# Optimization experiments

Hardware: AMD Instinct MI355X
Metric: run time of the kernel (lower is better)

## Reference

```python
import jax, jax.numpy as jnp
import numpy as np

N_NODES = 50000
N_EDGES = 800000
D = 64


def setup_inputs() -> dict:
    key = jax.random.key(0)
    k = jax.random.split(key, 8)
    h = jax.random.normal(k[0], (N_NODES, D), dtype=jnp.float32)
    edge_src = jax.random.randint(k[1], (N_EDGES,), 0, N_NODES, dtype=jnp.int32)
    edge_dst = jax.random.randint(k[2], (N_EDGES,), 0, N_NODES, dtype=jnp.int32)
    # normalized adjacency weights (e.g. 1/deg style values in (0,1))
    edge_w = jax.random.uniform(k[3], (N_EDGES,), dtype=jnp.float32)
    W_self = jax.random.normal(k[4], (D, D), dtype=jnp.float32) / np.sqrt(D)
    b_self = jnp.zeros((D,), dtype=jnp.float32)
    W_neigh = jax.random.normal(k[5], (D, D), dtype=jnp.float32) / np.sqrt(D)
    b_neigh = jnp.zeros((D,), dtype=jnp.float32)
    return {
        "h": h,
        "edge_src": edge_src,
        "edge_dst": edge_dst,
        "edge_w": edge_w,
        "W_self": W_self,
        "b_self": b_self,
        "W_neigh": W_neigh,
        "b_neigh": b_neigh,
    }


def reference(h, edge_src, edge_dst, edge_w, W_self, b_self, W_neigh, b_neigh):
    # neigh = A_norm @ h : sparse COO matmul as weighted gather + segment-sum
    # messages: [E, D]
    msgs = edge_w[:, None] * h[edge_src]
    neigh = jax.ops.segment_sum(msgs, edge_dst, num_segments=N_NODES)  # [N, D]
    # out = lin_self(h) + lin_neigh(neigh), relu; dropout is a no-op in eval mode
    out = (h @ W_self.T + b_self) + (neigh @ W_neigh.T + b_neigh)
    return jax.nn.relu(out)
```

## Files before the change

kernel.cpp:

```cpp
#include <hip/hip_runtime.h>

#define N_NODES 50000
#define N_EDGES 800000
#define D 64

#define NPB 200
#define NB  250
#define CAP 4096
#define BT  256
#define EPT 8
#define CHUNK_E (BT * EPT)
#define NCHUNKS ((N_EDGES + CHUNK_E - 1) / CHUNK_E)
#define CT  512

typedef unsigned short ushort_t;
typedef unsigned int   uint_t;

__device__ __forceinline__ ushort_t f2b(float f) {
    uint_t u = __float_as_uint(f);
    return (ushort_t)((u + 0x7FFFu + ((u >> 16) & 1u)) >> 16);
}
__device__ __forceinline__ float b2f(ushort_t b) {
    return __uint_as_float((uint_t)b << 16);
}


__global__ __launch_bounds__(256) void init_cursor_kernel(int* __restrict__ cursor)
{
    const int t = threadIdx.x;
    if (t < NB) cursor[t] = t * CAP;
}

__global__ __launch_bounds__(256) void h2b_kernel(
    const float* __restrict__ h, ushort_t* __restrict__ hb)
{
    const int i = blockIdx.x * 256 + threadIdx.x;
    if (i >= N_NODES * D / 4) return;
    const float4 v = ((const float4*)h)[i];
    ushort4 o;
    o.x = f2b(v.x); o.y = f2b(v.y); o.z = f2b(v.z); o.w = f2b(v.w);
    ((ushort4*)hb)[i] = o;
}

__global__ __launch_bounds__(BT) void bin_kernel(
    const int* __restrict__ src, const int* __restrict__ dst,
    const float* __restrict__ w, int* __restrict__ cursor,
    int2* __restrict__ bedges)
{
    __shared__ int lh[NB];
    __shared__ int loff[NB];
    __shared__ int lcur[NB];
    __shared__ int gpos[NB];
    __shared__ int part[256];
    __shared__ int2 stage[CHUNK_E];
    __shared__ unsigned char sbk[CHUNK_E];

    const int t = threadIdx.x;
    for (int i = t; i < NB; i += BT) lh[i] = 0;
    __syncthreads();

    const int base = blockIdx.x * CHUNK_E;
    int   my_b[EPT];
    int   my_p[EPT];
    float my_w[EPT];
#pragma unroll
    for (int k = 0; k < EPT; ++k) {
        const int e = base + k * BT + t;
        if (e < N_EDGES) {
            const int d = dst[e];
            const int b = (unsigned)d / NPB;
            my_b[k] = b;
            my_p[k] = (src[e] << 8) | (d - b * NPB);
            my_w[k] = w[e];
            atomicAdd(&lh[b], 1);
        } else {
            my_b[k] = -1;
        }
    }
    __syncthreads();

    const int v = (t < NB) ? lh[t] : 0;
    part[t] = v;
    __syncthreads();
    for (int off = 1; off < 256; off <<= 1) {
        int p = (t >= off) ? part[t - off] : 0;
        __syncthreads();
        part[t] += p;
        __syncthreads();
    }
    if (t < NB) { loff[t] = part[t] - v; lcur[t] = part[t] - v; }
    __syncthreads();

#pragma unroll
    for (int k = 0; k < EPT; ++k) {
        if (my_b[k] >= 0) {
            const int p = atomicAdd(&lcur[my_b[k]], 1);
            stage[p] = make_int2(my_p[k], __float_as_int(my_w[k]));
            sbk[p] = (unsigned char)my_b[k];
        }
    }
    __syncthreads();

    if (t < NB && lh[t] > 0) gpos[t] = atomicAdd(&cursor[t], lh[t]);
    __syncthreads();

    const int tot = min(N_EDGES - base, CHUNK_E);
    for (int s = t; s < tot; s += BT) {
        const int b = sbk[s];
        bedges[gpos[b] + (s - loff[b])] = stage[s];
    }
}

__global__ __launch_bounds__(CT) void bucket_csr_kernel(
    const int* __restrict__ cursor, int2* __restrict__ edges,
    int2* __restrict__ offs2)
{
    __shared__ int  lcur[NPB];
    __shared__ int  part[256];
    __shared__ int2 stage[CAP];

    const int b   = blockIdx.x;
    const int t   = threadIdx.x;
    const int gb  = b * CAP;
    const int cnt = min(cursor[b] - gb, CAP);

    if (t < NPB) lcur[t] = 0;
    __syncthreads();
    for (int e = t; e < cnt; e += CT)
        atomicAdd(&lcur[edges[gb + e].x & 255], 1);
    __syncthreads();

    const int v = (t < NPB) ? lcur[t] : 0;
    if (t < 256) part[t] = v;
    __syncthreads();
    for (int off = 1; off < 256; off <<= 1) {
        int p = (t >= off && t < 256) ? part[t - off] : 0;
        __syncthreads();
        if (t < 256) part[t] += p;
        __syncthreads();
    }
    if (t < NPB) {
        const int ex = part[t] - v;
        lcur[t] = ex;
        offs2[b * NPB + t] = make_int2(gb + ex, gb + ex + v);
    }
    __syncthreads();

    for (int e = t; e < cnt; e += CT) {
        const int2 r = edges[gb + e];
        const int p = atomicAdd(&lcur[r.x & 255], 1);
        stage[p] = make_int2(r.x >> 8, r.y);
    }
    __syncthreads();
    for (int s = t; s < cnt; s += CT)
        edges[gb + s] = stage[s];
}

__global__ __launch_bounds__(256) void gather_kernel(
    const ushort_t* __restrict__ hb, const int2* __restrict__ edges,
    const int2* __restrict__ offs2, ushort_t* __restrict__ neigh)
{
    const int node = (blockIdx.x * 256 + threadIdx.x) >> 6;
    const int lane = threadIdx.x & 63;
    if (node >= N_NODES) return;
    const int2 be = offs2[node];
    const int beg = be.x, end = be.y;
    float acc = 0.f;
    int e = beg;
    for (; e + 4 <= end; e += 4) {
        const int2 e0 = edges[e], e1 = edges[e + 1], e2 = edges[e + 2], e3 = edges[e + 3];
        const float v0 = b2f(hb[(size_t)e0.x * D + lane]);
        const float v1 = b2f(hb[(size_t)e1.x * D + lane]);
        const float v2 = b2f(hb[(size_t)e2.x * D + lane]);
        const float v3 = b2f(hb[(size_t)e3.x * D + lane]);
        acc = fmaf(__int_as_float(e0.y), v0, acc);
        acc = fmaf(__int_as_float(e1.y), v1, acc);
        acc = fmaf(__int_as_float(e2.y), v2, acc);
        acc = fmaf(__int_as_float(e3.y), v3, acc);
    }
    for (; e < end; ++e) {
        const int2 ed = edges[e];
        acc = fmaf(__int_as_float(ed.y), b2f(hb[(size_t)ed.x * D + lane]), acc);
    }
    neigh[(size_t)node * D + lane] = f2b(acc);
}

__device__ __forceinline__ float lane_bcast(float v, int l) {
    return __int_as_float(__builtin_amdgcn_readlane(__float_as_int(v), l));
}

__global__ __launch_bounds__(256, 2) void linear_bf_kernel(
    const ushort_t* __restrict__ hb, const ushort_t* __restrict__ neigh,
    const float* __restrict__ Ws, const float* __restrict__ bs,
    const float* __restrict__ Wn, const float* __restrict__ bn,
    float* __restrict__ out)
{
    const int lane   = threadIdx.x & 63;
    const int gwave  = (blockIdx.x * blockDim.x + threadIdx.x) >> 6;
    const int nwaves = (gridDim.x * blockDim.x) >> 6;

    float Wsr[D], Wnr[D];
#pragma unroll
    for (int k = 0; k < D; k += 4) {
        const float4 a = *(const float4*)&Ws[(size_t)lane * D + k];
        const float4 b = *(const float4*)&Wn[(size_t)lane * D + k];
        Wsr[k] = a.x; Wsr[k+1] = a.y; Wsr[k+2] = a.z; Wsr[k+3] = a.w;
        Wnr[k] = b.x; Wnr[k+1] = b.y; Wnr[k+2] = b.z; Wnr[k+3] = b.w;
    }
    const float bias = bs[lane] + bn[lane];

    for (int n = gwave; n < N_NODES; n += nwaves) {
        const float hv = b2f(hb[(size_t)n * D + lane]);
        const float nv = b2f(neigh[(size_t)n * D + lane]);
        float o = bias;
#pragma unroll
        for (int k = 0; k < D; ++k) {
            o = fmaf(lane_bcast(hv, k), Wsr[k], o);
            o = fmaf(lane_bcast(nv, k), Wnr[k], o);
        }
        out[(size_t)n * D + lane] = fmaxf(o, 0.f);
    }
}

__global__ __launch_bounds__(256) void sage_scatter(
    const float* __restrict__ h,
    const int* __restrict__ edge_src,
    const int* __restrict__ edge_dst,
    const float* __restrict__ edge_w,
    float* __restrict__ neigh)
{
    const long long tid = (long long)blockIdx.x * blockDim.x + threadIdx.x;
    const int e = (int)(tid >> 6);
    const int d = (int)(tid & 63);
    if (e >= N_EDGES) return;
    atomicAdd(&neigh[(long long)edge_dst[e] * D + d],
              edge_w[e] * h[(long long)edge_src[e] * D + d]);
}

__global__ __launch_bounds__(256, 2) void linear_f32_kernel(
    const float* __restrict__ h, const float* __restrict__ neigh,
    const float* __restrict__ Ws, const float* __restrict__ bs,
    const float* __restrict__ Wn, const float* __restrict__ bn,
    float* __restrict__ out)
{
    const int lane   = threadIdx.x & 63;
    const int gwave  = (blockIdx.x * blockDim.x + threadIdx.x) >> 6;
    const int nwaves = (gridDim.x * blockDim.x) >> 6;

    float Wsr[D], Wnr[D];
#pragma unroll
    for (int k = 0; k < D; k += 4) {
        const float4 a = *(const float4*)&Ws[(size_t)lane * D + k];
        const float4 b = *(const float4*)&Wn[(size_t)lane * D + k];
        Wsr[k] = a.x; Wsr[k+1] = a.y; Wsr[k+2] = a.z; Wsr[k+3] = a.w;
        Wnr[k] = b.x; Wnr[k+1] = b.y; Wnr[k+2] = b.z; Wnr[k+3] = b.w;
    }
    const float bias = bs[lane] + bn[lane];

    for (int n = gwave; n < N_NODES; n += nwaves) {
        const float hv = h[(size_t)n * D + lane];
        const float nv = neigh[(size_t)n * D + lane];
        float o = bias;
#pragma unroll
        for (int k = 0; k < D; ++k) {
            o = fmaf(lane_bcast(hv, k), Wsr[k], o);
            o = fmaf(lane_bcast(nv, k), Wnr[k], o);
        }
        out[(size_t)n * D + lane] = fmaxf(o, 0.f);
    }
}

extern "C" void kernel_launch(void* const* d_in, const int* in_sizes, int n_in,
                              void* d_out, int out_size, void* d_ws, size_t ws_size,
                              hipStream_t stream)
{
    const float* h        = (const float*)d_in[0];
    const int*   edge_src = (const int*)d_in[1];
    const int*   edge_dst = (const int*)d_in[2];
    const float* edge_w   = (const float*)d_in[3];
    const float* W_self   = (const float*)d_in[4];
    const float* b_self   = (const float*)d_in[5];
    const float* W_neigh  = (const float*)d_in[6];
    const float* b_neigh  = (const float*)d_in[7];
    float*       out      = (float*)d_out;

    int2*     edges  = (int2*)d_ws;
    int2*     offs2  = edges + (size_t)NB * CAP;
    ushort_t* hb     = (ushort_t*)(offs2 + N_NODES);
    ushort_t* neighb = hb + (size_t)N_NODES * D;
    int*      cursor = (int*)(neighb + (size_t)N_NODES * D);
    const size_t needed = (size_t)NB * CAP * 8 + (size_t)N_NODES * 8
                        + (size_t)N_NODES * D * 2 * 2 + NB * 4;

    if (ws_size >= needed) {
        init_cursor_kernel<<<1, 256, 0, stream>>>(cursor);
        h2b_kernel<<<(N_NODES * D / 4 + 255) / 256, 256, 0, stream>>>(h, hb);
        bin_kernel<<<NCHUNKS, BT, 0, stream>>>(edge_src, edge_dst, edge_w,
                                               cursor, edges);
        bucket_csr_kernel<<<NB, CT, 0, stream>>>(cursor, edges, offs2);
        gather_kernel<<<(N_NODES * 64 + 255) / 256, 256, 0, stream>>>(
            hb, edges, offs2, neighb);
        linear_bf_kernel<<<1024, 256, 0, stream>>>(hb, neighb, W_self, b_self,
                                                   W_neigh, b_neigh, out);
    } else {
        float* neigh_fb = (float*)d_ws;
        hipMemsetAsync(neigh_fb, 0, (size_t)N_NODES * D * sizeof(float), stream);
        const long long total = (long long)N_EDGES * 64;
        sage_scatter<<<(int)((total + 255) / 256), 256, 0, stream>>>(
            h, edge_src, edge_dst, edge_w, neigh_fb);
        linear_f32_kernel<<<1024, 256, 0, stream>>>(h, neigh_fb, W_self, b_self,
                                                    W_neigh, b_neigh, out);
    }
}
```

Measured before the change: 173.6 us.

## Fold cursor init into h2b, enlarge bin/CSR blocks, unroll gather by 8

Removes the separate cursor-initialisation launch by having block 0 of the bf16 conversion kernel set the bucket cursors. It changes the binning kernel to 512 threads with 4 edges per thread and the CSR bucket kernel to 1024 threads, guarding the 256-wide scan for the larger blocks. It also adds an 8-way unrolled loop in the gather kernel so more independent row loads are in flight per node. Larger blocks may reduce occupancy, and the extra unrolling raises register use.

```diff
diff --git a/kernel.cpp b/kernel.cpp
--- a/kernel.cpp
+++ b/kernel.cpp
@@ -7,11 +7,11 @@
 #define NPB 200
 #define NB  250
 #define CAP 4096
-#define BT  256
-#define EPT 8
+#define BT  512
+#define EPT 4
 #define CHUNK_E (BT * EPT)
 #define NCHUNKS ((N_EDGES + CHUNK_E - 1) / CHUNK_E)
-#define CT  512
+#define CT  1024
 
 typedef unsigned short ushort_t;
 typedef unsigned int   uint_t;
@@ -25,15 +25,11 @@
 }
 
 
-__global__ __launch_bounds__(256) void init_cursor_kernel(int* __restrict__ cursor)
-{
-    const int t = threadIdx.x;
-    if (t < NB) cursor[t] = t * CAP;
-}
-
 __global__ __launch_bounds__(256) void h2b_kernel(
-    const float* __restrict__ h, ushort_t* __restrict__ hb)
-{
+    const float* __restrict__ h, ushort_t* __restrict__ hb,
+    int* __restrict__ cursor)
+{
+    if (blockIdx.x == 0 && threadIdx.x < NB) cursor[threadIdx.x] = threadIdx.x * CAP;
     const int i = blockIdx.x * 256 + threadIdx.x;
     if (i >= N_NODES * D / 4) return;
     const float4 v = ((const float4*)h)[i];
@@ -80,12 +76,13 @@
     __syncthreads();
 
     const int v = (t < NB) ? lh[t] : 0;
-    part[t] = v;
+    if (t < 256) part[t] = v;
     __syncthreads();
     for (int off = 1; off < 256; off <<= 1) {
-        int p = (t >= off) ? part[t - off] : 0;
+        int p = 0;
+        if (t < 256 && t >= off) p = part[t - off];
         __syncthreads();
-        part[t] += p;
+        if (t < 256) part[t] += p;
         __syncthreads();
     }
     if (t < NB) { loff[t] = part[t] - v; lcur[t] = part[t] - v; }
@@ -134,7 +131,8 @@
     if (t < 256) part[t] = v;
     __syncthreads();
     for (int off = 1; off < 256; off <<= 1) {
-        int p = (t >= off && t < 256) ? part[t - off] : 0;
+        int p = 0;
+        if (t < 256 && t >= off) p = part[t - off];
         __syncthreads();
         if (t < 256) part[t] += p;
         __syncthreads();
@@ -167,6 +165,16 @@
     const int beg = be.x, end = be.y;
     float acc = 0.f;
     int e = beg;
+    for (; e + 8 <= end; e += 8) {
+        int2  r[8];
+        float vv[8];
+#pragma unroll
+        for (int k = 0; k < 8; ++k) r[k] = edges[e + k];
+#pragma unroll
+        for (int k = 0; k < 8; ++k) vv[k] = b2f(hb[(size_t)r[k].x * D + lane]);
+#pragma unroll
+        for (int k = 0; k < 8; ++k) acc = fmaf(__int_as_float(r[k].y), vv[k], acc);
+    }
     for (; e + 4 <= end; e += 4) {
         const int2 e0 = edges[e], e1 = edges[e + 1], e2 = edges[e + 2], e3 = edges[e + 3];
         const float v0 = b2f(hb[(size_t)e0.x * D + lane]);
@@ -293,8 +301,7 @@
                         + (size_t)N_NODES * D * 2 * 2 + NB * 4;
 
     if (ws_size >= needed) {
-        init_cursor_kernel<<<1, 256, 0, stream>>>(cursor);
-        h2b_kernel<<<(N_NODES * D / 4 + 255) / 256, 256, 0, stream>>>(h, hb);
+        h2b_kernel<<<(N_NODES * D / 4 + 255) / 256, 256, 0, stream>>>(h, hb, cursor);
         bin_kernel<<<NCHUNKS, BT, 0, stream>>>(edge_src, edge_dst, edge_w,
                                                cursor, edges);
         bucket_csr_kernel<<<NB, CT, 0, stream>>>(cursor, edges, offs2);
```

After: 167.6 us. 3.5% less time.
